# Optimization experiments

Hardware: AMD Instinct MI355X
Metric: run time of the kernel (lower is better)

## Reference

```python
import jax, jax.numpy as jnp
import numpy as np

B, N, F = 32, 256, 12          # batch, Nc, in_dim
E_IN, E_H, E_OUT, N_OUT = 2 * (F + 1) + 6, 32, 30, 12


def setup_inputs() -> dict:
    key = jax.random.key(0)
    ks = jax.random.split(key, 12)
    x = jax.random.normal(ks[0], (B, N, F), jnp.float32)
    d = jax.random.uniform(ks[1], (B, N, N), jnp.float32, 0.1, 10.0)
    mask = jax.random.uniform(ks[2], (B, N, N)) > 0.3
    adj_dist = jnp.where(mask, d, 0.0)
    adj_direct = jax.random.uniform(ks[3], (B, N, N), jnp.float32, 0.0, 2.0 * np.pi)
    wind_mean = jax.random.normal(ks[4], (B, 2), jnp.float32)
    wind_std = jax.random.uniform(ks[5], (B, 2), jnp.float32, 0.5, 1.5)
    s = 0.1
    W1 = jax.random.normal(ks[6], (E_IN, E_H), jnp.float32) * s
    b1 = jnp.zeros((E_H,), jnp.float32)
    W2 = jax.random.normal(ks[7], (E_H, E_OUT), jnp.float32) * s
    b2 = jnp.zeros((E_OUT,), jnp.float32)
    W3 = jax.random.normal(ks[8], (E_OUT, N_OUT), jnp.float32) * s
    b3 = jnp.zeros((N_OUT,), jnp.float32)
    return {"x": x, "adj_dist": adj_dist, "adj_direct": adj_direct,
            "wind_mean": wind_mean, "wind_std": wind_std,
            "W1": W1, "b1": b1, "W2": W2, "b2": b2, "W3": W3, "b3": b3}


def reference(x, adj_dist, adj_direct, wind_mean, wind_std, W1, b1, W2, b2, W3, b3):
    # adj mask: edge exists where adj_dist != 0  -> (B,N,N,1)
    a = (adj_dist != 0).astype(x.dtype)[..., None]
    # broadcast-gather src/target node features onto all pairs, masked, +edge flag
    node_src = jnp.concatenate([a * x[:, :, None, :], a], axis=-1)   # (B,N,N,F+1)
    node_tgt = jnp.concatenate([a * x[:, None, :, :], a], axis=-1)   # (B,N,N,F+1)
    # normalize dist/direction over (batch, src) dims; torch .std is unbiased
    dist = adj_dist[..., None]
    direc = adj_direct[..., None]
    dist_n = (dist - dist.mean(axis=(0, 1))) / dist.std(axis=(0, 1), ddof=1)
    direc_n = (direc - direc.mean(axis=(0, 1))) / direc.std(axis=(0, 1), ddof=1)
    # edge feature tensor (B,N,N,32) = 2*(F+1) + 6
    out0 = jnp.concatenate(
        [node_src, node_tgt, dist_n, a, direc_n, a, a, a], axis=-1)
    # tiny edge MLP (sigmoid-sigmoid)
    h = jax.nn.sigmoid(out0 @ W1 + b1)
    e = jax.nn.sigmoid(h @ W2 + b2)                                  # (B,N,N,E_OUT)
    # aggregate: sum over src rows (incoming) minus sum over dest cols (outgoing)
    agg = e.sum(axis=1) - e.sum(axis=2)                              # (B,N,E_OUT)
    # node MLP
    return jax.nn.sigmoid(agg @ W3 + b3)                             # (B,N,N_OUT)
```

## Files before the change

kernel.cpp:

```cpp
#include <hip/hip_runtime.h>
#include <hip/hip_bf16.h>
#include <math.h>

#define BB 32
#define NN 256
#define FF 12
#define WS_SUMS   0
#define WS_STATS  1024
#define WS_W2P    2048
#define WS_B2P    3072
#define WS_USG    4096
#define WS_UTPG   (WS_USG + 262144)
#define WS_MIN    (WS_UTPG + 262144)
#define WS_PLUS   (WS_MIN + 262144)

typedef __attribute__((ext_vector_type(8))) short bf16x8;
typedef __attribute__((ext_vector_type(4))) float f32x4;

__device__ __forceinline__ float sig(float x) {
    return __builtin_amdgcn_rcpf(1.0f + __expf(-x));
}
__device__ __forceinline__ short f2bf(float x) {
    __hip_bfloat16 b = __float2bfloat16(x);
    short s; __builtin_memcpy(&s, &b, 2); return s;
}
__device__ __forceinline__ float bf2f(short s) {
    __hip_bfloat16 b; __builtin_memcpy(&b, &s, 2);
    return __bfloat162float(b);
}

__global__ __launch_bounds__(256) void colstats_kernel(
    const float* __restrict__ dist, const float* __restrict__ direc, float* __restrict__ sums)
{
    const int t = threadIdx.x;
    const int r0 = blockIdx.x * 32;
    float sd = 0.f, sdd = 0.f, sr = 0.f, srr = 0.f;
    for (int rr = 0; rr < 32; ++rr) {
        const float d  = dist [(r0 + rr) * NN + t];
        const float dr = direc[(r0 + rr) * NN + t];
        sd += d;  sdd = fmaf(d, d, sdd);
        sr += dr; srr = fmaf(dr, dr, srr);
    }
    atomicAdd(&sums[t],        sd);
    atomicAdd(&sums[256 + t],  sdd);
    atomicAdd(&sums[512 + t],  sr);
    atomicAdd(&sums[768 + t],  srr);
}

__global__ __launch_bounds__(256) void finalize_kernel(
    const float* __restrict__ sums, const float* __restrict__ W2, const float* __restrict__ b2,
    float* __restrict__ stats, float* __restrict__ W2p, float* __restrict__ b2p)
{
    const int t = threadIdx.x;
    const float M = (float)(BB * NN);
    {   const float s = sums[t], q = sums[256 + t];
        const float mean = s / M;
        float var = (q - s * mean) / (M - 1.0f);
        if (var < 1e-20f) var = 1e-20f;
        stats[t] = mean; stats[256 + t] = rsqrtf(var);
    }
    {   const float s = sums[512 + t], q = sums[768 + t];
        const float mean = s / M;
        float var = (q - s * mean) / (M - 1.0f);
        if (var < 1e-20f) var = 1e-20f;
        stats[512 + t] = mean; stats[768 + t] = rsqrtf(var);
    }
    for (int idx = t; idx < 1024; idx += 256) {
        const int k = idx >> 5, m = idx & 31;
        W2p[idx] = (m < 30) ? W2[k * 30 + m] : 0.0f;
    }
    if (t < 32) b2p[t] = (t < 30) ? b2[t] : 0.0f;
}

__global__ __launch_bounds__(256) void node_pre_kernel(
    const float* __restrict__ x, const float* __restrict__ W1, const float* __restrict__ b1,
    float* __restrict__ usg, float* __restrict__ utpg)
{
    const int idx = blockIdx.x * 256 + threadIdx.x;
    const int r = idx >> 5, k = idx & 31;
    const float* xr = x + r * FF;
    float us = 0.f, ut = 0.f;
#pragma unroll
    for (int f = 0; f < FF; ++f) {
        const float xv = xr[f];
        us = fmaf(xv, W1[f * 32 + k], us);
        ut = fmaf(xv, W1[(13 + f) * 32 + k], ut);
    }
    const float ca = W1[12 * 32 + k] + W1[25 * 32 + k] + W1[27 * 32 + k]
                   + W1[29 * 32 + k] + W1[30 * 32 + k] + W1[31 * 32 + k];
    usg[idx]  = us;
    utpg[idx] = ut + ca + b1[k];
}

__global__ __launch_bounds__(256, 2) void edge_mfma_kernel(
    const float* __restrict__ adj_dist, const float* __restrict__ adj_direct,
    const float* __restrict__ W1, const float* __restrict__ b1,
    const float* __restrict__ usg, const float* __restrict__ utpg,
    const float* __restrict__ stats, const float* __restrict__ W2p,
    const float* __restrict__ b2p, float* __restrict__ plus,
    float* __restrict__ minusv, int lognit)
{
    __shared__ float us_s[64][32];
    __shared__ float pool[8192];
    float (*mins)[4][32] = reinterpret_cast<float(*)[4][32]>(pool);
    float (*ldst)[257]   = reinterpret_cast<float(*)[257]>(pool);

    const int t    = threadIdx.x;
    const int nit  = 1 << lognit;
    const int R    = NN >> lognit;
    const int b    = blockIdx.x >> lognit;
    const int it   = blockIdx.x & (nit - 1);
    const int i0   = it * R;
    const int w    = t >> 6;
    const int l    = t & 63;
    const int m0   = l & 15;
    const int g    = l >> 4;
    const int kb   = g << 3;

    { const int k = t & 31;
      for (int ii = t >> 5; ii < R; ii += 8)
          us_s[ii][k] = usg[((b << 8) + i0 + ii) * 32 + k]; }
    __syncthreads();

    float b1c[8], r26c[8], r28c[8];
#pragma unroll
    for (int e = 0; e < 8; ++e) {
        b1c[e]  = b1[kb + e];
        r26c[e] = W1[26 * 32 + kb + e];
        r28c[e] = W1[28 * 32 + kb + e];
    }
    float utpc[4][8];
#pragma unroll
    for (int jt = 0; jt < 4; ++jt) {
        const int j = (w << 6) + m0 + (jt << 4);
        const float4* uv = (const float4*)(utpg + ((b << 8) + j) * 32 + kb);
        float4 a0 = uv[0], a1 = uv[1];
        utpc[jt][0]=a0.x; utpc[jt][1]=a0.y; utpc[jt][2]=a0.z; utpc[jt][3]=a0.w;
        utpc[jt][4]=a1.x; utpc[jt][5]=a1.y; utpc[jt][6]=a1.z; utpc[jt][7]=a1.w;
    }
    float mdp[4], isdp[4], mrp[4], isrp[4];
#pragma unroll
    for (int jt = 0; jt < 4; ++jt) {
        const int j = (w << 6) + m0 + (jt << 4);
        mdp[jt] = stats[j];        isdp[jt] = stats[256 + j];
        mrp[jt] = stats[512 + j];  isrp[jt] = stats[768 + j];
    }
    bf16x8 whi[2], wlo[2];
#pragma unroll
    for (int mt = 0; mt < 2; ++mt) {
        const int m = m0 + (mt << 4);
#pragma unroll
        for (int e = 0; e < 8; ++e) {
            const float wv = W2p[(kb + e) * 32 + m];
            const short h16 = f2bf(wv);
            whi[mt][e] = h16;
            wlo[mt][e] = f2bf(wv - bf2f(h16));
        }
    }
    const float b2c[2] = { b2p[m0], b2p[m0 + 16] };
    const bool mt1ok = (m0 < 14);

    float accp[4][2][4];
#pragma unroll
    for (int jt = 0; jt < 4; ++jt)
#pragma unroll
        for (int mt = 0; mt < 2; ++mt)
#pragma unroll
            for (int r = 0; r < 4; ++r) accp[jt][mt][r] = 0.0f;

    const float* dptr = adj_dist   + (((b << 8) + i0) << 8) + t;
    const float* rptr = adj_direct + (((b << 8) + i0) << 8) + t;
    float dN = dptr[0], rN = rptr[0];

#pragma unroll 1
    for (int i = 0; i < R; ++i) {
        const float dcur = dN, rcur = rN;
        if (i + 1 < R) { dN = dptr[(i + 1) << 8]; rN = rptr[(i + 1) << 8]; }

        float usc[8];
        { const float4* uv = (const float4*)&us_s[i][kb];
          float4 a0 = uv[0], a1 = uv[1];
          usc[0]=a0.x; usc[1]=a0.y; usc[2]=a0.z; usc[3]=a0.w;
          usc[4]=a1.x; usc[5]=a1.y; usc[6]=a1.z; usc[7]=a1.w; }

        bf16x8 afr[4];
#pragma unroll
        for (int jt = 0; jt < 4; ++jt) {
            const float dv = __shfl(dcur, m0 + (jt << 4));
            const float rv = __shfl(rcur, m0 + (jt << 4));
            const bool  a  = (dv != 0.0f);
            const float dn = (dv - mdp[jt]) * isdp[jt];
            const float rn = (rv - mrp[jt]) * isrp[jt];
#pragma unroll
            for (int e = 0; e < 8; ++e) {
                float z = a ? (usc[e] + utpc[jt][e]) : b1c[e];
                z = fmaf(dn, r26c[e], z);
                z = fmaf(rn, r28c[e], z);
                afr[jt][e] = f2bf(sig(z));
            }
        }

        float msum0 = 0.0f, msum1 = 0.0f;
#pragma unroll
        for (int jt = 0; jt < 4; ++jt) {
#pragma unroll
            for (int mt = 0; mt < 2; ++mt) {
                f32x4 d4 = {0.f, 0.f, 0.f, 0.f};
                d4 = __builtin_amdgcn_mfma_f32_16x16x32_bf16(afr[jt], wlo[mt], d4, 0, 0, 0);
                d4 = __builtin_amdgcn_mfma_f32_16x16x32_bf16(afr[jt], whi[mt], d4, 0, 0, 0);
#pragma unroll
                for (int r = 0; r < 4; ++r) {
                    float e = sig(d4[r] + b2c[mt]);
                    if (mt == 1 && !mt1ok) e = 0.0f;
                    accp[jt][mt][r] += e;
                    if (mt == 0) msum0 += e; else msum1 += e;
                }
            }
        }
        msum0 += __shfl_xor(msum0, 16); msum0 += __shfl_xor(msum0, 32);
        msum1 += __shfl_xor(msum1, 16); msum1 += __shfl_xor(msum1, 32);
        if (l < 16) { mins[i][w][l] = msum0; mins[i][w][l + 16] = msum1; }
    }
    __syncthreads();

    { const int m = t & 31;
      if (m < 30)
          for (int ii = t >> 5; ii < R; ii += 8) {
              const float s = mins[ii][0][m] + mins[ii][1][m]
                            + mins[ii][2][m] + mins[ii][3][m];
              minusv[((b << 5) + m) * 256 + i0 + ii] = s;
          } }
    __syncthreads();

#pragma unroll
    for (int jt = 0; jt < 4; ++jt)
#pragma unroll
        for (int mt = 0; mt < 2; ++mt) {
            const int m = m0 + (mt << 4);
            if (m < 30) {
#pragma unroll
                for (int r = 0; r < 4; ++r) {
                    const int j = (w << 6) + (jt << 4) + (g << 2) + r;
                    ldst[m][j] = accp[jt][mt][r];
                }
            }
        }
    __syncthreads();
    { const int base = ((b << lognit) + it) << 13;
#pragma unroll
      for (int m = 0; m < 30; ++m)
          plus[base + (m << 8) + t] = ldst[m][t];
    }
}

__global__ __launch_bounds__(256) void reduce_out_kernel(
    const float* __restrict__ plus, const float* __restrict__ minusv,
    const float* __restrict__ W3, const float* __restrict__ b3,
    float* __restrict__ out, int lognit)
{
    const int b = blockIdx.x;
    const int n = threadIdx.x;
    const int nit = 1 << lognit;

    float acc[30];
#pragma unroll
    for (int m = 0; m < 30; ++m) acc[m] = -minusv[((b << 5) + m) * 256 + n];
#pragma unroll 1
    for (int it = 0; it < nit; ++it) {
        const float* p = plus + (((b << lognit) + it) << 13) + n;
#pragma unroll
        for (int m = 0; m < 30; ++m) acc[m] += p[m << 8];
    }
    float* op = out + ((b << 8) + n) * 12;
#pragma unroll
    for (int o = 0; o < 12; ++o) {
        float z = b3[o];
#pragma unroll
        for (int m = 0; m < 30; ++m) z = fmaf(acc[m], W3[m * 12 + o], z);
        op[o] = sig(z);
    }
}

extern "C" void kernel_launch(void* const* d_in, const int* in_sizes, int n_in,
                              void* d_out, int out_size, void* d_ws, size_t ws_size,
                              hipStream_t stream)
{
    const float* x    = (const float*)d_in[0];
    const float* adjd = (const float*)d_in[1];
    const float* adjr = (const float*)d_in[2];
    const float* W1   = (const float*)d_in[5];
    const float* b1   = (const float*)d_in[6];
    const float* W2   = (const float*)d_in[7];
    const float* b2   = (const float*)d_in[8];
    const float* W3   = (const float*)d_in[9];
    const float* b3   = (const float*)d_in[10];
    float* ws  = (float*)d_ws;
    float* out = (float*)d_out;

    int lognit = 2;
    if      (ws_size >= ((size_t)WS_PLUS + 16u * 262144u) * 4u) lognit = 4;
    else if (ws_size >= ((size_t)WS_PLUS +  8u * 262144u) * 4u) lognit = 3;

    hipMemsetAsync(ws + WS_SUMS, 0, 1024 * sizeof(float), stream);

    colstats_kernel<<<256, 256, 0, stream>>>(adjd, adjr, ws + WS_SUMS);
    node_pre_kernel<<<1024, 256, 0, stream>>>(x, W1, b1, ws + WS_USG, ws + WS_UTPG);
    finalize_kernel<<<1, 256, 0, stream>>>(ws + WS_SUMS, W2, b2,
                                           ws + WS_STATS, ws + WS_W2P, ws + WS_B2P);
    edge_mfma_kernel<<<BB << lognit, 256, 0, stream>>>(adjd, adjr, W1, b1,
                                                       ws + WS_USG, ws + WS_UTPG,
                                                       ws + WS_STATS, ws + WS_W2P,
                                                       ws + WS_B2P, ws + WS_PLUS,
                                                       ws + WS_MIN, lognit);
    reduce_out_kernel<<<BB, 256, 0, stream>>>(ws + WS_PLUS, ws + WS_MIN,
                                              W3, b3, out, lognit);
}
```

Measured before the change: 166.3 us.

## Split edge kernel across column halves and widen reduce-out grid

Each edge block now handles one half of the destination columns, which doubles the grid and lets occupancy rise to four blocks per SIMD via launch bounds. Per-thread register arrays shrink, and the minus sums are written per half and combined in the reduce kernel. The reduce kernel uses 8x more blocks, staging aggregates in shared memory before the node MLP. Also folds b2 into the MFMA accumulator init, packs bf16 by truncation instead of round-to-nearest, and unrolls colstats; the truncation slightly changes numerics.

```diff
diff --git a/kernel.cpp b/kernel.cpp
--- a/kernel.cpp
+++ b/kernel.cpp
@@ -10,9 +10,9 @@
 #define WS_W2P    2048
 #define WS_B2P    3072
 #define WS_USG    4096
-#define WS_UTPG   (WS_USG + 262144)
-#define WS_MIN    (WS_UTPG + 262144)
-#define WS_PLUS   (WS_MIN + 262144)
+#define WS_UTPG   266240
+#define WS_MIN    528384
+#define WS_PLUS   1052672
 
 typedef __attribute__((ext_vector_type(8))) short bf16x8;
 typedef __attribute__((ext_vector_type(4))) float f32x4;
@@ -28,6 +28,11 @@
     __hip_bfloat16 b; __builtin_memcpy(&b, &s, 2);
     return __bfloat162float(b);
 }
+__device__ __forceinline__ unsigned pkbf(float lo, float hi) {
+    unsigned ulo, uhi;
+    __builtin_memcpy(&ulo, &lo, 4); __builtin_memcpy(&uhi, &hi, 4);
+    return (uhi & 0xffff0000u) | (ulo >> 16);
+}
 
 __global__ __launch_bounds__(256) void colstats_kernel(
     const float* __restrict__ dist, const float* __restrict__ direc, float* __restrict__ sums)
@@ -35,6 +40,7 @@
     const int t = threadIdx.x;
     const int r0 = blockIdx.x * 32;
     float sd = 0.f, sdd = 0.f, sr = 0.f, srr = 0.f;
+#pragma unroll 4
     for (int rr = 0; rr < 32; ++rr) {
         const float d  = dist [(r0 + rr) * NN + t];
         const float dr = direc[(r0 + rr) * NN + t];
@@ -92,7 +98,7 @@
     utpg[idx] = ut + ca + b1[k];
 }
 
-__global__ __launch_bounds__(256, 2) void edge_mfma_kernel(
+__global__ __launch_bounds__(256, 4) void edge_mfma_kernel(
     const float* __restrict__ adj_dist, const float* __restrict__ adj_direct,
     const float* __restrict__ W1, const float* __restrict__ b1,
     const float* __restrict__ usg, const float* __restrict__ utpg,
@@ -103,19 +109,22 @@
     __shared__ float us_s[64][32];
     __shared__ float pool[8192];
     float (*mins)[4][32] = reinterpret_cast<float(*)[4][32]>(pool);
-    float (*ldst)[257]   = reinterpret_cast<float(*)[257]>(pool);
+    float (*ldst)[129]   = reinterpret_cast<float(*)[129]>(pool);
 
     const int t    = threadIdx.x;
     const int nit  = 1 << lognit;
     const int R    = NN >> lognit;
-    const int b    = blockIdx.x >> lognit;
-    const int it   = blockIdx.x & (nit - 1);
+    const int bid  = blockIdx.x;
+    const int b    = bid >> (lognit + 1);
+    const int it   = (bid >> 1) & (nit - 1);
+    const int jh   = bid & 1;
     const int i0   = it * R;
     const int w    = t >> 6;
     const int l    = t & 63;
     const int m0   = l & 15;
     const int g    = l >> 4;
     const int kb   = g << 3;
+    const int jbase = (jh << 7) + (w << 5);
 
     { const int k = t & 31;
       for (int ii = t >> 5; ii < R; ii += 8)
@@ -129,19 +138,19 @@
         r26c[e] = W1[26 * 32 + kb + e];
         r28c[e] = W1[28 * 32 + kb + e];
     }
-    float utpc[4][8];
-#pragma unroll
-    for (int jt = 0; jt < 4; ++jt) {
-        const int j = (w << 6) + m0 + (jt << 4);
+    float utpc[2][8];
+#pragma unroll
+    for (int jt = 0; jt < 2; ++jt) {
+        const int j = jbase + (jt << 4) + m0;
         const float4* uv = (const float4*)(utpg + ((b << 8) + j) * 32 + kb);
         float4 a0 = uv[0], a1 = uv[1];
         utpc[jt][0]=a0.x; utpc[jt][1]=a0.y; utpc[jt][2]=a0.z; utpc[jt][3]=a0.w;
         utpc[jt][4]=a1.x; utpc[jt][5]=a1.y; utpc[jt][6]=a1.z; utpc[jt][7]=a1.w;
     }
-    float mdp[4], isdp[4], mrp[4], isrp[4];
-#pragma unroll
-    for (int jt = 0; jt < 4; ++jt) {
-        const int j = (w << 6) + m0 + (jt << 4);
+    float mdp[2], isdp[2], mrp[2], isrp[2];
+#pragma unroll
+    for (int jt = 0; jt < 2; ++jt) {
+        const int j = jbase + (jt << 4) + m0;
         mdp[jt] = stats[j];        isdp[jt] = stats[256 + j];
         mrp[jt] = stats[512 + j];  isrp[jt] = stats[768 + j];
     }
@@ -160,16 +169,17 @@
     const float b2c[2] = { b2p[m0], b2p[m0 + 16] };
     const bool mt1ok = (m0 < 14);
 
-    float accp[4][2][4];
-#pragma unroll
-    for (int jt = 0; jt < 4; ++jt)
+    float accp[2][2][4];
+#pragma unroll
+    for (int jt = 0; jt < 2; ++jt)
 #pragma unroll
         for (int mt = 0; mt < 2; ++mt)
 #pragma unroll
             for (int r = 0; r < 4; ++r) accp[jt][mt][r] = 0.0f;
 
-    const float* dptr = adj_dist   + (((b << 8) + i0) << 8) + t;
-    const float* rptr = adj_direct + (((b << 8) + i0) << 8) + t;
+    const int col = (jh << 7) + (w << 5) + (l & 31);
+    const float* dptr = adj_dist   + (((b << 8) + i0) << 8) + col;
+    const float* rptr = adj_direct + (((b << 8) + i0) << 8) + col;
     float dN = dptr[0], rN = rptr[0];
 
 #pragma unroll 1
@@ -183,34 +193,40 @@
           usc[0]=a0.x; usc[1]=a0.y; usc[2]=a0.z; usc[3]=a0.w;
           usc[4]=a1.x; usc[5]=a1.y; usc[6]=a1.z; usc[7]=a1.w; }
 
-        bf16x8 afr[4];
-#pragma unroll
-        for (int jt = 0; jt < 4; ++jt) {
-            const float dv = __shfl(dcur, m0 + (jt << 4));
-            const float rv = __shfl(rcur, m0 + (jt << 4));
+        bf16x8 afr[2];
+#pragma unroll
+        for (int jt = 0; jt < 2; ++jt) {
+            const int src = (jt << 4) + m0;
+            const float dv = __shfl(dcur, src);
+            const float rv = __shfl(rcur, src);
             const bool  a  = (dv != 0.0f);
             const float dn = (dv - mdp[jt]) * isdp[jt];
             const float rn = (rv - mrp[jt]) * isrp[jt];
+            float h[8];
 #pragma unroll
             for (int e = 0; e < 8; ++e) {
                 float z = a ? (usc[e] + utpc[jt][e]) : b1c[e];
                 z = fmaf(dn, r26c[e], z);
                 z = fmaf(rn, r28c[e], z);
-                afr[jt][e] = f2bf(sig(z));
+                h[e] = sig(z);
             }
+            union { bf16x8 v; unsigned u[4]; } af;
+#pragma unroll
+            for (int p = 0; p < 4; ++p) af.u[p] = pkbf(h[2*p], h[2*p+1]);
+            afr[jt] = af.v;
         }
 
         float msum0 = 0.0f, msum1 = 0.0f;
 #pragma unroll
-        for (int jt = 0; jt < 4; ++jt) {
+        for (int jt = 0; jt < 2; ++jt) {
 #pragma unroll
             for (int mt = 0; mt < 2; ++mt) {
-                f32x4 d4 = {0.f, 0.f, 0.f, 0.f};
+                f32x4 d4 = { b2c[mt], b2c[mt], b2c[mt], b2c[mt] };
                 d4 = __builtin_amdgcn_mfma_f32_16x16x32_bf16(afr[jt], wlo[mt], d4, 0, 0, 0);
                 d4 = __builtin_amdgcn_mfma_f32_16x16x32_bf16(afr[jt], whi[mt], d4, 0, 0, 0);
 #pragma unroll
                 for (int r = 0; r < 4; ++r) {
-                    float e = sig(d4[r] + b2c[mt]);
+                    float e = sig(d4[r]);
                     if (mt == 1 && !mt1ok) e = 0.0f;
                     accp[jt][mt][r] += e;
                     if (mt == 0) msum0 += e; else msum1 += e;
@@ -228,28 +244,31 @@
           for (int ii = t >> 5; ii < R; ii += 8) {
               const float s = mins[ii][0][m] + mins[ii][1][m]
                             + mins[ii][2][m] + mins[ii][3][m];
-              minusv[((b << 5) + m) * 256 + i0 + ii] = s;
+              minusv[((b * 2 + jh) * 32 + m) * 256 + i0 + ii] = s;
           } }
     __syncthreads();
 
 #pragma unroll
-    for (int jt = 0; jt < 4; ++jt)
+    for (int jt = 0; jt < 2; ++jt)
 #pragma unroll
         for (int mt = 0; mt < 2; ++mt) {
             const int m = m0 + (mt << 4);
             if (m < 30) {
 #pragma unroll
                 for (int r = 0; r < 4; ++r) {
-                    const int j = (w << 6) + (jt << 4) + (g << 2) + r;
-                    ldst[m][j] = accp[jt][mt][r];
+                    const int jl = (w << 5) + (jt << 4) + (g << 2) + r;
+                    ldst[m][jl] = accp[jt][mt][r];
                 }
             }
         }
     __syncthreads();
     { const int base = ((b << lognit) + it) << 13;
-#pragma unroll
-      for (int m = 0; m < 30; ++m)
-          plus[base + (m << 8) + t] = ldst[m][t];
+      const int jl = t & 127;
+#pragma unroll
+      for (int mi = 0; mi < 15; ++mi) {
+          const int m = (mi << 1) + (t >> 7);
+          plus[base + (m << 8) + (jh << 7) + jl] = ldst[m][jl];
+      }
     }
 }
 
@@ -258,26 +277,38 @@
     const float* __restrict__ W3, const float* __restrict__ b3,
     float* __restrict__ out, int lognit)
 {
-    const int b = blockIdx.x;
-    const int n = threadIdx.x;
+    __shared__ float agg_s[32][33];
+    const int b   = blockIdx.x >> 3;
+    const int nh  = blockIdx.x & 7;
+    const int t   = threadIdx.x;
+    const int nl  = t & 31;
+    const int n   = (nh << 5) + nl;
+    const int mg  = t >> 5;
     const int nit = 1 << lognit;
 
-    float acc[30];
-#pragma unroll
-    for (int m = 0; m < 30; ++m) acc[m] = -minusv[((b << 5) + m) * 256 + n];
+    float acc[4] = {0.f, 0.f, 0.f, 0.f};
 #pragma unroll 1
     for (int it = 0; it < nit; ++it) {
         const float* p = plus + (((b << lognit) + it) << 13) + n;
 #pragma unroll
-        for (int m = 0; m < 30; ++m) acc[m] += p[m << 8];
-    }
-    float* op = out + ((b << 8) + n) * 12;
-#pragma unroll
-    for (int o = 0; o < 12; ++o) {
+        for (int q = 0; q < 4; ++q) acc[q] += p[((mg << 2) + q) << 8];
+    }
+#pragma unroll
+    for (int q = 0; q < 4; ++q) {
+        const int m = (mg << 2) + q;
+        float v = acc[q]
+                - minusv[((b * 2 + 0) * 32 + m) * 256 + n]
+                - minusv[((b * 2 + 1) * 32 + m) * 256 + n];
+        agg_s[nl][m] = (m < 30) ? v : 0.0f;
+    }
+    __syncthreads();
+
+    for (int task = t; task < 384; task += 256) {
+        const int n2 = task / 12, o = task % 12;
         float z = b3[o];
 #pragma unroll
-        for (int m = 0; m < 30; ++m) z = fmaf(acc[m], W3[m * 12 + o], z);
-        op[o] = sig(z);
+        for (int m = 0; m < 30; ++m) z = fmaf(agg_s[n2][m], W3[m * 12 + o], z);
+        out[(((b << 8) + (nh << 5) + n2) * 12) + o] = sig(z);
     }
 }
 
@@ -307,11 +338,11 @@
     node_pre_kernel<<<1024, 256, 0, stream>>>(x, W1, b1, ws + WS_USG, ws + WS_UTPG);
     finalize_kernel<<<1, 256, 0, stream>>>(ws + WS_SUMS, W2, b2,
                                            ws + WS_STATS, ws + WS_W2P, ws + WS_B2P);
-    edge_mfma_kernel<<<BB << lognit, 256, 0, stream>>>(adjd, adjr, W1, b1,
-                                                       ws + WS_USG, ws + WS_UTPG,
-                                                       ws + WS_STATS, ws + WS_W2P,
-                                                       ws + WS_B2P, ws + WS_PLUS,
-                                                       ws + WS_MIN, lognit);
-    reduce_out_kernel<<<BB, 256, 0, stream>>>(ws + WS_PLUS, ws + WS_MIN,
-                                              W3, b3, out, lognit);
-}
+    edge_mfma_kernel<<<BB << (lognit + 1), 256, 0, stream>>>(adjd, adjr, W1, b1,
+                                                             ws + WS_USG, ws + WS_UTPG,
+                                                             ws + WS_STATS, ws + WS_W2P,
+                                                             ws + WS_B2P, ws + WS_PLUS,
+                                                             ws + WS_MIN, lognit);
+    reduce_out_kernel<<<BB * 8, 256, 0, stream>>>(ws + WS_PLUS, ws + WS_MIN,
+                                                  W3, b3, out, lognit);
+}
```

After: 149.8 us. -9.9%, faster.
